# Performance work log

Measured on AMD Instinct MI355X. Metric: run time of the kernel, lower is better.

Reference implementation:

```python
import jax, jax.numpy as jnp
import numpy as np

NS = [65536, 16384, 4096, 1024, 256, 64]          # nodes per level (64 = 8 graphs x 8 dense voxels)
ES = [1048576, 262144, 65536, 16384, 4096]        # edges per level (avg degree 16)
INS = [1, 15, 23, 31, 39]
OUTS = [12, 20, 28, 36, 44]
K = 5                                             # kernel_size


def setup_inputs():
    keys = iter(jax.random.split(jax.random.key(0), 64))
    d = {'x': jax.random.normal(next(keys), (NS[0], 1), jnp.float32),
         'pos': jax.random.uniform(next(keys), (NS[0], 3), jnp.float32)}
    for l in range(5):
        n, e, ci, co = NS[l], ES[l], INS[l], OUTS[l]
        d[f'src{l}'] = jax.random.randint(next(keys), (e,), 0, n)
        d[f'dst{l}'] = jax.random.randint(next(keys), (e,), 0, n)
        d[f'eattr{l}'] = jax.random.normal(next(keys), (e, 3), jnp.float32)
        d[f'cluster{l}'] = jax.random.randint(next(keys), (n,), 0, NS[l + 1])
        d[f'w1_{l}'] = jax.random.normal(next(keys), (3, K), jnp.float32) * 0.5
        d[f'b1_{l}'] = jnp.zeros((K,), jnp.float32)
        d[f'w2_{l}'] = jax.random.normal(next(keys), (K, ci * co), jnp.float32) / np.float32(np.sqrt(K * ci))
        d[f'b2_{l}'] = jnp.zeros((ci * co,), jnp.float32)
        d[f'root_{l}'] = jax.random.normal(next(keys), (ci, co), jnp.float32) / np.float32(np.sqrt(ci))
        d[f'bias_{l}'] = jnp.zeros((co,), jnp.float32)
    d['fc_w'] = jax.random.normal(next(keys), (8 * 47, 10), jnp.float32) / np.float32(np.sqrt(8 * 47))
    d['fc_b'] = jnp.zeros((10,), jnp.float32)
    return d


def _conv(x, src, dst, eattr, w1, b1, w2, b2, root, bias, n):
    # edge-conditioned kernel: MLP(edge_attr) -> [E, ci, co]
    h = jnp.tanh(eattr @ w1 + b1)                                  # [E, K]
    We = (h @ w2 + b2).reshape(eattr.shape[0], x.shape[1], -1)     # [E, ci, co]
    msg = jnp.einsum('ei,eio->eo', x[src], We)                     # gather + per-edge matvec
    s = jax.ops.segment_sum(msg, dst, num_segments=n)
    cnt = jax.ops.segment_sum(jnp.ones((dst.shape[0], 1), x.dtype), dst, num_segments=n)
    agg = s / jnp.maximum(cnt, 1.0)                                # mean aggregation
    return agg + x @ root + bias, jnp.mean(jnp.square(We))


def _pool(x, pos, cluster, n_next):
    # sparse voxel max pool on features, mean on positions; pos concatenated to features
    xm = jax.ops.segment_max(x, cluster, num_segments=n_next)
    xm = jnp.where(jnp.isfinite(xm), xm, 0.0)                      # empty voxels -> 0
    ps = jax.ops.segment_sum(pos, cluster, num_segments=n_next)
    cnt = jax.ops.segment_sum(jnp.ones((pos.shape[0], 1), pos.dtype), cluster, num_segments=n_next)
    pm = ps / jnp.maximum(cnt, 1.0)
    return jnp.concatenate([xm, pm], axis=1), pm


def reference(x, pos, src0, dst0, eattr0, cluster0, w1_0, b1_0, w2_0, b2_0, root_0, bias_0,
              src1, dst1, eattr1, cluster1, w1_1, b1_1, w2_1, b2_1, root_1, bias_1,
              src2, dst2, eattr2, cluster2, w1_2, b1_2, w2_2, b2_2, root_2, bias_2,
              src3, dst3, eattr3, cluster3, w1_3, b1_3, w2_3, b2_3, root_3, bias_3,
              src4, dst4, eattr4, cluster4, w1_4, b1_4, w2_4, b2_4, root_4, bias_4,
              fc_w, fc_b):
    lv = [(src0, dst0, eattr0, cluster0, w1_0, b1_0, w2_0, b2_0, root_0, bias_0),
          (src1, dst1, eattr1, cluster1, w1_1, b1_1, w2_1, b2_1, root_1, bias_1),
          (src2, dst2, eattr2, cluster2, w1_2, b1_2, w2_2, b2_2, root_2, bias_2),
          (src3, dst3, eattr3, cluster3, w1_3, b1_3, w2_3, b2_3, root_3, bias_3),
          (src4, dst4, eattr4, cluster4, w1_4, b1_4, w2_4, b2_4, root_4, bias_4)]
    closs = jnp.float32(0.0)
    for l, (src, dst, ea, cl, w1, b1, w2, b2, rt, bs) in enumerate(lv):
        x, c = _conv(x, src, dst, ea, w1, b1, w2, b2, rt, bs, NS[l])
        closs = closs + c
        x, pos = _pool(x, pos, cl, NS[l + 1])
    feat = x.reshape(-1, 8 * 47)                                   # [B, 8*47]
    logits = feat @ fc_w + fc_b
    return jax.nn.log_softmax(logits, axis=1), closs
```

## Files before the change

kernel.cpp:

```cpp
#include <hip/hip_runtime.h>
#include <hip/hip_fp16.h>
#include <math.h>


#define TILES1 256
#define TSZ1   1024
#define NB1    512
#define NBUK   1024
#define CAP0   1280

__device__ __forceinline__ float ftanh(float x) {
    float e = __expf(2.f * x);
    return 1.f - 2.f / (e + 1.f);
}

__device__ __forceinline__ unsigned fenc(float f) {
    int b = __float_as_int(f);
    return (b < 0) ? ~(unsigned)b : ((unsigned)b | 0x80000000u);
}
__device__ __forceinline__ float fdec(unsigned u) {
    int b = (u & 0x80000000u) ? (int)(u & 0x7fffffffu) : ~(int)u;
    return __int_as_float(b);
}

__device__ __forceinline__ float row_val(const unsigned* __restrict__ row,
                                         int i, int CI) {
    float cn = __uint_as_float(row[CI]);
    if (i < CI - 3) return (cn == 0.f) ? 0.f : fdec(row[i]);
    return __uint_as_float(row[i]) / fmaxf(cn, 1.f);
}

struct Seg4 {
    const int* idx[4];
    int*       cnt[4];
    int*       rp [4];
    int*       out[4];
    int        n  [4];
    int        nb [4];
    int        tstart[5];
};

struct GA {
    const int *src0, *dst0; const float* ea0;
    const int *src1, *dst1; const float* ea1;
    const float *x0, *pos0;
    const int* cluster[5];
    const float *w1[5], *b1[5], *w2[5], *b2[5], *root[5], *bias[5];
    const int* srcE[3]; const float* eaE[3];
    const float *fc_w, *fc_b;
    int* bcnt;
    float4* pay2;
    float* y0;
    float* xn0;
    unsigned* raw[5];
    float* H; float* sq;
    int *M1, *M21, *bktTot, *bs1;
    float4 *pay1, *rec1; int* rp1;
    Seg4 sg;
    float* out;
    const float* hea[4]; int hE[4]; int hb0[5];
    int hsB;
};

__global__ __launch_bounds__(256) void k1_fuseA(GA A)
{
    __shared__ int sh[NBUK];
    int B = blockIdx.x, t = threadIdx.x;

    if (B < 1024) {
        for (int u = t; u < NBUK; u += 256) sh[u] = 0;
        __syncthreads();
        int base = B * 1024 + t;
        int dreg[4];
        #pragma unroll
        for (int it = 0; it < 4; it++) {
            dreg[it] = A.dst0[base + it * 256];
            atomicAdd(&sh[dreg[it] >> 6], 1);
        }
        __syncthreads();
        for (int u = t; u < NBUK; u += 256) {
            int c = sh[u];
            sh[u] = c ? atomicAdd(&A.bcnt[u], c) : 0;
        }
        __syncthreads();
        float w1r[15], b1r[5];
        #pragma unroll
        for (int i = 0; i < 15; i++) w1r[i] = A.w1[0][i];
        #pragma unroll
        for (int i = 0; i < 5; i++)  b1r[i] = A.b1[0][i];
        float acc[20];
        #pragma unroll
        for (int i = 0; i < 20; i++) acc[i] = 0.f;
        #pragma unroll
        for (int it = 0; it < 4; it++) {
            int i = base + it * 256;
            int d = dreg[it];
            int sv = A.src0[i];
            float e0 = A.ea0[i * 3], e1 = A.ea0[i * 3 + 1], e2 = A.ea0[i * 3 + 2];
            float h[5];
            #pragma unroll
            for (int k = 0; k < 5; k++)
                h[k] = ftanh(e0 * w1r[k] + e1 * w1r[5 + k] + e2 * w1r[10 + k] + b1r[k]);
            int p = 5;
            #pragma unroll
            for (int k = 0; k < 5; k++) {
                acc[k] += h[k];
                #pragma unroll
                for (int k2 = k; k2 < 5; k2++) acc[p++] += h[k] * h[k2];
            }
            float xv = A.x0[sv];
            union HU { __half2 h2; float f; } p01, p23;
            p01.h2 = __floats2half2_rn(h[0], h[1]);
            p23.h2 = __floats2half2_rn(h[2], h[3]);
            unsigned wbits = ((unsigned)d << 16) |
                             (unsigned)__half_as_ushort(__float2half_rn(h[4]));
            int bk = d >> 6;
            int ps = atomicAdd(&sh[bk], 1);
            if (ps < CAP0)
                A.pay2[(size_t)bk * CAP0 + ps] =
                    make_float4(xv, p01.f, p23.f, __uint_as_float(wbits));
        }
        __syncthreads();
        float* red = (float*)sh;
        int wid = t >> 6, lane = t & 63;
        #pragma unroll
        for (int v = 0; v < 20; v++) {
            float s = acc[v];
            #pragma unroll
            for (int o = 32; o; o >>= 1) s += __shfl_down(s, o);
            if (lane == 0) red[wid * 20 + v] = s;
        }
        __syncthreads();
        if (t < 20)
            atomicAdd(&A.H[t], red[t] + red[20 + t] + red[40 + t] + red[60 + t]);
        return;
    }
    B -= 1024;
    if (B < TILES1) {
        for (int u = t; u < NB1; u += 256) sh[u] = 0;
        __syncthreads();
        int base = B * TSZ1 + t;
        #pragma unroll
        for (int it = 0; it < 4; it++)
            atomicAdd(&sh[A.dst1[base + it * 256] >> 5], 1);
        __syncthreads();
        for (int u = t; u < NB1; u += 256) {
            int c = sh[u];
            A.M1[(size_t)B * NB1 + u] = c;
            if (c) atomicAdd(&A.bktTot[u], c);
        }
        return;
    }
    B -= TILES1;
    if (B < A.hsB) {
        const int K = 8;
        int j = 0;
        while (j < 3 && B >= A.hb0[j + 1]) j++;
        int bloc = B - A.hb0[j];
        const float* ea = A.hea[j];
        const float* w1p = A.w1[j + 1];
        const float* b1p = A.b1[j + 1];
        float w1r[15], b1r[5];
        #pragma unroll
        for (int i = 0; i < 15; i++) w1r[i] = w1p[i];
        #pragma unroll
        for (int i = 0; i < 5; i++)  b1r[i] = b1p[i];
        float acc[20];
        #pragma unroll
        for (int i = 0; i < 20; i++) acc[i] = 0.f;
        int base = bloc * 256 * K + t;
        for (int it = 0; it < K; it++) {
            int e = base + it * 256;
            if (e < A.hE[j]) {
                float e0 = ea[e * 3], e1 = ea[e * 3 + 1], e2 = ea[e * 3 + 2];
                float h[5];
                #pragma unroll
                for (int k = 0; k < 5; k++)
                    h[k] = ftanh(e0 * w1r[k] + e1 * w1r[5 + k] + e2 * w1r[10 + k] + b1r[k]);
                int p = 5;
                #pragma unroll
                for (int k = 0; k < 5; k++) {
                    acc[k] += h[k];
                    #pragma unroll
                    for (int k2 = k; k2 < 5; k2++) acc[p++] += h[k] * h[k2];
                }
            }
        }
        float* red = (float*)sh;
        int wid = t >> 6, lane = t & 63;
        #pragma unroll
        for (int v = 0; v < 20; v++) {
            float s = acc[v];
            #pragma unroll
            for (int o = 32; o; o >>= 1) s += __shfl_down(s, o);
            if (lane == 0) red[wid * 20 + v] = s;
        }
        __syncthreads();
        if (t < 20)
            atomicAdd(&A.H[(j + 1) * 20 + t],
                      red[t] + red[20 + t] + red[40 + t] + red[60 + t]);
        return;
    }
    B -= A.hsB;
    {
        int s = 0;
        while (s < 3 && B >= A.sg.tstart[s + 1]) s++;
        int i0 = (B - A.sg.tstart[s]) * 1024;
        const int* idx = A.sg.idx[s];
        int* cnt = A.sg.cnt[s];
        int n = A.sg.n[s];
        #pragma unroll
        for (int j = 0; j < 4; j++) {
            int i = i0 + j * 256 + t;
            if (i < n) atomicAdd(&cnt[idx[i]], 1);
        }
    }
}

__global__ __launch_bounds__(256) void k2_fuseB(GA A)
{
    __shared__ int sc[256];
    __shared__ float wsm[96];
    __shared__ float nacc[7 * 64];
    int B = blockIdx.x, t = threadIdx.x;

    if (B < NBUK) {
        if (t < 60) wsm[t] = A.w2[0][t];
        else if (t >= 64  && t < 76)  wsm[60 + t - 64]  = A.b2[0][t - 64];
        else if (t >= 128 && t < 140) wsm[72 + t - 128] = A.root[0][t - 128];
        else if (t >= 192 && t < 204) wsm[84 + t - 192] = A.bias[0][t - 192];
        for (int u = t; u < 7 * 64; u += 256) nacc[u] = 0.f;
        __syncthreads();

        int n = A.bcnt[B];
        if (n > CAP0) n = CAP0;
        size_t base = (size_t)B * CAP0;
        for (int j = t; j < n; j += 256) {
            float4 R = A.pay2[base + j];
            union HU { float f; __half2 h2; } a01, a23;
            a01.f = R.y; a23.f = R.z;
            unsigned wbits = __float_as_uint(R.w);
            int rel = (int)(wbits >> 16) & 63;
            float xv = R.x;
            atomicAdd(&nacc[rel], xv);
            atomicAdd(&nacc[64 + rel],  __low2float(a01.h2)  * xv);
            atomicAdd(&nacc[128 + rel], __high2float(a01.h2) * xv);
            atomicAdd(&nacc[192 + rel], __low2float(a23.h2)  * xv);
            atomicAdd(&nacc[256 + rel], __high2float(a23.h2) * xv);
            atomicAdd(&nacc[320 + rel],
                      __half2float(__ushort_as_half((unsigned short)(wbits & 0xffffu))) * xv);
            atomicAdd(&nacc[384 + rel], 1.f);
        }
        __syncthreads();

        int v0 = B << 6;
        for (int u = t; u < 64 * 12; u += 256) {
            int rel = u / 12, o = u - rel * 12;
            float dg = nacc[384 + rel];
            float inv = 1.f / fmaxf(dg, 1.f);
            float msg = wsm[60 + o] * nacc[rel] + wsm[o] * nacc[64 + rel] +
                        wsm[12 + o] * nacc[128 + rel] + wsm[24 + o] * nacc[192 + rel] +
                        wsm[36 + o] * nacc[256 + rel] + wsm[48 + o] * nacc[320 + rel];
            float xv = A.x0[v0 + rel];
            A.y0[(size_t)(v0 + rel) * 12 + o] =
                msg * inv + xv * wsm[72 + o] + wsm[84 + o];
        }
        return;
    }
    B -= NBUK;
    if (B < NB1) {
        int v = A.M1[(size_t)t * NB1 + B];
        sc[t] = v;
        __syncthreads();
        for (int d = 1; d < 256; d <<= 1) {
            int u = (t >= d) ? sc[t - d] : 0;
            __syncthreads();
            sc[t] += u;
            __syncthreads();
        }
        A.M21[(size_t)t * NB1 + B] = sc[t] - v;
        return;
    }
    B -= NB1;
    if (B < 1) {
        int a0 = A.bktTot[2 * t], a1 = A.bktTot[2 * t + 1];
        int ps = a0 + a1;
        sc[t] = ps;
        __syncthreads();
        for (int d = 1; d < 256; d <<= 1) {
            int u = (t >= d) ? sc[t - d] : 0;
            __syncthreads();
            sc[t] += u;
            __syncthreads();
        }
        int excl = sc[t] - ps;
        A.bs1[2 * t]     = excl;
        A.bs1[2 * t + 1] = excl + a0;
        if (t == 255) A.bs1[512] = sc[255];
        return;
    }
    B -= 1;
    if (B < 4) {
        int s = B;
        int nb = A.sg.nb[s];
        const int* cnt = A.sg.cnt[s];
        int* rp = A.sg.rp[s];
        int VPT = nb >> 8;
        int i0 = t * VPT;
        int sum = 0;
        for (int k = 0; k < VPT; k++) sum += cnt[i0 + k];
        int acc = sum;
        sc[t] = acc;
        __syncthreads();
        for (int d = 1; d < 256; d <<= 1) {
            int t2 = (t >= d) ? sc[t - d] : 0;
            __syncthreads();
            acc += t2;
            sc[t] = acc;
            __syncthreads();
        }
        int running = acc - sum;
        for (int k = 0; k < VPT; k++) {
            rp[i0 + k] = running;
            running += cnt[i0 + k];
        }
        if (t == 255) rp[nb] = running;
        return;
    }
    B -= 4;
    {
        if (t >= 64) return;
        int l = B;
        const float* w2l = A.w2[l];
        const float* b2l = A.b2[l];
        static const int cicoA[5] = {12, 300, 644, 1116, 1716};
        int cico = cicoA[l];
        float d[21];
        #pragma unroll
        for (int i = 0; i < 21; i++) d[i] = 0.f;
        for (int u = t; u < cico; u += 64) {
            float b = b2l[u];
            float w[5];
            #pragma unroll
            for (int k = 0; k < 5; k++) w[k] = w2l[k * cico + u];
            int p = 0;
            #pragma unroll
            for (int k = 0; k < 5; k++) {
                #pragma unroll
                for (int k2 = k; k2 < 5; k2++) d[p++] += w[k] * w[k2];
            }
            #pragma unroll
            for (int k = 0; k < 5; k++) d[15 + k] += b * w[k];
            d[20] += b * b;
        }
        #pragma unroll
        for (int i = 0; i < 21; i++) {
            #pragma unroll
            for (int off = 32; off; off >>= 1) d[i] += __shfl_down(d[i], off);
        }
        if (t == 0) {
            static const int EA[5] = {1048576, 262144, 65536, 16384, 4096};
            const float* H1 = A.H + l * 20;
            const float* H2 = H1 + 5;
            float sq = (float)EA[l] * d[20];
            #pragma unroll
            for (int k = 0; k < 5; k++) sq += 2.f * d[15 + k] * H1[k];
            int p = 0;
            #pragma unroll
            for (int k = 0; k < 5; k++) {
                #pragma unroll
                for (int k2 = k; k2 < 5; k2++) {
                    sq += ((k == k2) ? 1.f : 2.f) * d[p] * H2[p];
                    p++;
                }
            }
            A.sq[l] = sq;
        }
    }
}

__global__ __launch_bounds__(256) void k3_fuseC(GA A)
{
    __shared__ int shi[NB1];
    int B = blockIdx.x, t = threadIdx.x;

    if (B < TILES1) {
        int tile = B;
        for (int u = t; u < NB1; u += 256)
            shi[u] = A.bs1[u] + A.M21[(size_t)tile * NB1 + u];
        __syncthreads();
        int base = tile * TSZ1 + t;
        #pragma unroll
        for (int it = 0; it < 4; it++) {
            int i = base + it * 256;
            int d = A.dst1[i];
            int key = (d << 16) | A.src1[i];
            float e0 = A.ea1[i * 3], e1 = A.ea1[i * 3 + 1], e2 = A.ea1[i * 3 + 2];
            int ps = atomicAdd(&shi[d >> 5], 1);
            A.pay1[ps] = make_float4(__int_as_float(key), e0, e1, e2);
        }
        return;
    }
    B -= TILES1;
    {
        int s = 0;
        while (s < 3 && B >= A.sg.tstart[s + 1]) s++;
        int i0 = (B - A.sg.tstart[s]) * 1024;
        const int* idx = A.sg.idx[s];
        int* cnt = A.sg.cnt[s];
        const int* rp = A.sg.rp[s];
        int* out = A.sg.out[s];
        int n = A.sg.n[s];
        #pragma unroll
        for (int j = 0; j < 4; j++) {
            int i = i0 + j * 256 + t;
            if (i < n) {
                int d = idx[i];
                int p = atomicSub(&cnt[d], 1) - 1;
                out[rp[d] + p] = i;
            }
        }
    }
}

__global__ __launch_bounds__(256) void k4_fuseD(GA A)
{
    __shared__ int hist[32], cur[32];
    int B = blockIdx.x, t = threadIdx.x;

    if (B < NB1) {
        int b = B;
        int lo = A.bs1[b], hi = A.bs1[b + 1];
        int bin0 = b << 5;
        if (t < 32) hist[t] = 0;
        __syncthreads();
        const float* payw = (const float*)A.pay1;
        for (int j = lo + t; j < hi; j += 256) {
            int rel = (int)(__float_as_uint(payw[4 * j]) >> 16) - bin0;
            atomicAdd(&hist[rel], 1);
        }
        __syncthreads();
        if (t < 32) {
            int v = hist[t];
            int val = v;
            #pragma unroll
            for (int d = 1; d < 32; d <<= 1) {
                int u = __shfl_up(val, d);
                if (t >= d) val += u;
            }
            cur[t] = lo + val - v;
            A.rp1[bin0 + t] = lo + val - v;
            if (b == NB1 - 1 && t == 31) A.rp1[NB1 * 32] = hi;
        }
        __syncthreads();
        for (int j = lo + t; j < hi; j += 256) {
            float4 R = A.pay1[j];
            int rel = (int)(__float_as_uint(R.x) >> 16) - bin0;
            int p = atomicAdd(&cur[rel], 1);
            A.rec1[p] = R;
        }
        return;
    }
    B -= NB1;
    {
        int gt = B * 256 + t;
        if (gt >= 16384 * 15) return;
        int c = gt / 15, o = gt - c * 15;
        int r0 = A.sg.rp[3][c], r1 = A.sg.rp[3][c + 1];
        const int* cnid = A.sg.out[3];
        int d = r1 - r0;
        if (o < 12) {
            float m = -INFINITY;
            for (int j = r0; j < r1; j++)
                m = fmaxf(m, A.y0[(size_t)cnid[j] * 12 + o]);
            if (d == 0 || !isfinite(m)) m = 0.f;
            A.xn0[c * 15 + o] = m;
        } else {
            int k = o - 12;
            float sum = 0.f;
            for (int j = r0; j < r1; j++)
                sum += A.pos0[cnid[j] * 3 + k];
            A.xn0[c * 15 + o] = sum / fmaxf((float)d, 1.f);
        }
    }
}

__global__ __launch_bounds__(256) void k5_conv1(GA A)
{
    constexpr int CI = 15, CO = 20, CH = 48, CICO = CI * CO, RN = 24;
    __shared__ float w1s[20];
    __shared__ float4 recb[CH];
    __shared__ int   svb[CH];
    __shared__ float hb[CH * 6];
    __shared__ float xs[CH * CI];
    __shared__ float Sx[6 * CI];
    __shared__ float xown[CI];

    int t = threadIdx.x, v = blockIdx.x;
    if (t < 20) w1s[t] = (t < 15) ? A.w1[1][t] : A.b1[1][t - 15];
    if (t < CI) xown[t] = A.xn0[v * CI + t];
    int r0 = A.rp1[v], r1 = A.rp1[v + 1];
    int d = r1 - r0;
    float acc = 0.f;

    for (int c0 = r0; c0 < r1; c0 += CH) {
        int cn = min(CH, r1 - c0);
        if (t < cn) {
            float4 R = A.rec1[c0 + t];
            recb[t] = R;
            svb[t]  = (int)(__float_as_uint(R.x) & 0xffffu);
            hb[t * 6] = 1.f;
        }
        __syncthreads();
        if (t < cn * 5) {
            int j = t / 5, k = t % 5;
            float e0 = recb[j].y, e1 = recb[j].z, e2 = recb[j].w;
            hb[j * 6 + 1 + k] =
                ftanh(e0 * w1s[k] + e1 * w1s[5 + k] + e2 * w1s[10 + k] + w1s[15 + k]);
        }
        for (int u = t; u < cn * CI; u += 256) {
            int j = u / CI, i = u - j * CI;
            xs[u] = A.xn0[svb[j] * CI + i];
        }
        __syncthreads();
        if (t < 6 * CI) {
            int i = t / 6, k6 = t - (t / 6) * 6;
            for (int j = 0; j < cn; j++)
                acc += hb[j * 6 + k6] * xs[j * CI + i];
        }
        __syncthreads();
    }

    if (t < 6 * CI) Sx[t] = acc;
    __syncthreads();

    if (t < CO) {
        float m = 0.f;
        const float* w2 = A.w2[1];
        const float* b2 = A.b2[1];
        for (int i = 0; i < CI; i++) {
            m += b2[i * CO + t] * Sx[i * 6];
            #pragma unroll
            for (int k = 0; k < 5; k++)
                m += w2[k * CICO + i * CO + t] * Sx[i * 6 + 1 + k];
        }
        m /= fmaxf((float)d, 1.f);
        for (int i = 0; i < CI; i++) m += xown[i] * A.root[1][i * CO + t];
        m += A.bias[1][t];
        int c = A.cluster[1][v];
        unsigned* orow = A.raw[1] + (size_t)c * RN;
        atomicMax(&orow[t], fenc(m));
        if (t < 3) atomicAdd((float*)&orow[CO + t], xown[CI - 3 + t]);
        if (t == 0) atomicAdd((float*)&orow[CO + 3], 1.f);
    }
}

template<int CI, int CO>
__global__ __launch_bounds__(256) void coopP_k(GA A, int l)
{
    constexpr int CH = 48, CICO = CI * CO, RL = CI + 1, RN = CO + 4;
    __shared__ float w1s[20];
    __shared__ int   eb[CH], svb[CH];
    __shared__ float hb[CH * 6];
    __shared__ float xs[CH * CI];
    __shared__ float Sx[6 * CI];
    __shared__ float xown[CI];

    int t = threadIdx.x, v = blockIdx.x;
    int s = l - 2;
    const unsigned* rin = A.raw[l - 1];
    const int* rp = A.sg.rp[s];
    const int* eid = A.sg.out[s];
    const int* src = A.srcE[s];
    const float* eattr = A.eaE[s];

    if (t < 20) w1s[t] = (t < 15) ? A.w1[l][t] : A.b1[l][t - 15];
    if (t < CI) xown[t] = row_val(rin + (size_t)v * RL, t, CI);
    int r0 = rp[v], r1 = rp[v + 1];
    int d = r1 - r0;
    float acc = 0.f;

    for (int c0 = r0; c0 < r1; c0 += CH) {
        int cn = min(CH, r1 - c0);
        if (t < cn) {
            int e = eid[c0 + t];
            eb[t]  = e;
            svb[t] = src[e];
            hb[t * 6] = 1.f;
        }
        __syncthreads();
        if (t < cn * 5) {
            int j = t / 5, k = t % 5;
            int e = eb[j];
            float e0 = eattr[e * 3], e1 = eattr[e * 3 + 1], e2 = eattr[e * 3 + 2];
            hb[j * 6 + 1 + k] =
                ftanh(e0 * w1s[k] + e1 * w1s[5 + k] + e2 * w1s[10 + k] + w1s[15 + k]);
        }
        for (int u = t; u < cn * CI; u += 256) {
            int j = u / CI, i = u - j * CI;
            xs[u] = row_val(rin + (size_t)svb[j] * RL, i, CI);
        }
        __syncthreads();
        if (t < 6 * CI) {
            int i = t / 6, k6 = t - (t / 6) * 6;
            for (int j = 0; j < cn; j++)
                acc += hb[j * 6 + k6] * xs[j * CI + i];
        }
        __syncthreads();
    }

    if (t < 6 * CI) Sx[t] = acc;
    __syncthreads();

    if (t < CO) {
        float m = 0.f;
        const float* w2 = A.w2[l];
        const float* b2 = A.b2[l];
        for (int i = 0; i < CI; i++) {
            m += b2[i * CO + t] * Sx[i * 6];
            #pragma unroll
            for (int k = 0; k < 5; k++)
                m += w2[k * CICO + i * CO + t] * Sx[i * 6 + 1 + k];
        }
        m /= fmaxf((float)d, 1.f);
        for (int i = 0; i < CI; i++) m += xown[i] * A.root[l][i * CO + t];
        m += A.bias[l][t];
        int c = A.cluster[l][v];
        unsigned* orow = A.raw[l] + (size_t)c * RN;
        atomicMax(&orow[t], fenc(m));
        if (t < 3) atomicAdd((float*)&orow[CO + t], xown[CI - 3 + t]);
        if (t == 0) atomicAdd((float*)&orow[CO + 3], 1.f);
    }
}

__global__ __launch_bounds__(128) void k9_fc(GA A)
{
    __shared__ float feat[8 * 376];
    __shared__ float logit[80];
    __shared__ float roff[8];
    const unsigned* r5 = A.raw[4];
    for (int idx = threadIdx.x; idx < 64 * 47; idx += 128) {
        int n = idx / 47, i = idx - n * 47;
        int b = n >> 3, s = n & 7;
        feat[b * 376 + s * 47 + i] = row_val(r5 + (size_t)n * 48, i, 47);
    }
    __syncthreads();
    int t = threadIdx.x;
    if (t < 80) {
        int b = t / 10, j = t % 10;
        float acc = A.fc_b[j];
        for (int k = 0; k < 376; k++) acc += feat[b * 376 + k] * A.fc_w[k * 10 + j];
        logit[t] = acc;
    }
    __syncthreads();
    if (t < 8) {
        float m = -1e30f;
        for (int j = 0; j < 10; j++) m = fmaxf(m, logit[t * 10 + j]);
        float ssum = 0.f;
        for (int j = 0; j < 10; j++) ssum += expf(logit[t * 10 + j] - m);
        roff[t] = m + logf(ssum);
    }
    __syncthreads();
    if (t < 80) A.out[t] = logit[t] - roff[t / 10];
    if (t == 0) {
        const float* sq = A.sq;
        float closs = 0.f;
        closs += sq[0] * (1.0f / 12582912.0f);
        closs += sq[1] * (1.0f / 78643200.0f);
        closs += sq[2] * (1.0f / 42205184.0f);
        closs += sq[3] * (1.0f / 18284544.0f);
        closs += sq[4] * (1.0f / 7028736.0f);
        A.out[80] = closs;
    }
}


extern "C" void kernel_launch(void* const* d_in, const int* in_sizes, int n_in,
                              void* d_out, int out_size, void* d_ws, size_t ws_size,
                              hipStream_t stream)
{
    static const int NSa[6] = {65536, 16384, 4096, 1024, 256, 64};
    static const int ESa[5] = {1048576, 262144, 65536, 16384, 4096};
    static const int RNa[5] = {16, 24, 32, 40, 48};

    int* wsw = (int*)d_ws;
    size_t off = 0;
    auto alw = [&](size_t n) -> size_t {
        size_t p = off; off += (n + 63) & ~(size_t)63; return p;
    };
    size_t degO[5];
    for (int l = 2; l < 5; l++) degO[l] = alw(NSa[l]);
    size_t cdeg0O = alw(NSa[1]);
    size_t HO   = alw(100);
    size_t bcO  = alw(NBUK);
    size_t btO  = alw(NB1);
    size_t rawO[5];
    for (int l = 1; l < 5; l++) rawO[l] = alw((size_t)NSa[l + 1] * RNa[l]);
    size_t zeroWords = off;
    size_t rpO[5], eidO[5];
    for (int l = 2; l < 5; l++) rpO[l]  = alw(NSa[l] + 1);
    size_t crp0O = alw(NSa[1] + 1);
    for (int l = 2; l < 5; l++) eidO[l] = alw(ESa[l]);
    size_t cnid0O = alw(NSa[0]);
    size_t pay2O = alw((size_t)NBUK * CAP0 * 4);
    size_t y0O   = alw((size_t)NSa[0] * 12);
    size_t xn0O  = alw((size_t)NSa[1] * 15);
    size_t M1O   = alw((size_t)TILES1 * NB1);
    size_t M21O  = alw((size_t)TILES1 * NB1);
    size_t bs1O  = alw(NB1 + 1);
    size_t pay1O = alw((size_t)ESa[1] * 4);
    size_t rec1O = alw((size_t)ESa[1] * 4);
    size_t rp1O  = alw(NSa[1] + 1);
    size_t sqO   = alw(8);

    GA A{};
    A.src0 = (const int*)d_in[2];  A.dst0 = (const int*)d_in[3];
    A.ea0  = (const float*)d_in[4];
    A.src1 = (const int*)d_in[12]; A.dst1 = (const int*)d_in[13];
    A.ea1  = (const float*)d_in[14];
    A.x0   = (const float*)d_in[0];
    A.pos0 = (const float*)d_in[1];
    for (int l = 0; l < 5; l++) {
        A.cluster[l] = (const int*)d_in[5 + 10 * l];
        A.w1[l]   = (const float*)d_in[6 + 10 * l];
        A.b1[l]   = (const float*)d_in[7 + 10 * l];
        A.w2[l]   = (const float*)d_in[8 + 10 * l];
        A.b2[l]   = (const float*)d_in[9 + 10 * l];
        A.root[l] = (const float*)d_in[10 + 10 * l];
        A.bias[l] = (const float*)d_in[11 + 10 * l];
    }
    for (int s = 0; s < 3; s++) {
        A.srcE[s] = (const int*)d_in[2 + 10 * (s + 2)];
        A.eaE[s]  = (const float*)d_in[4 + 10 * (s + 2)];
    }
    A.fc_w = (const float*)d_in[52];
    A.fc_b = (const float*)d_in[53];
    A.bcnt = wsw + bcO;
    A.pay2 = (float4*)(wsw + pay2O);
    A.y0   = (float*)(wsw + y0O);
    A.xn0  = (float*)(wsw + xn0O);
    for (int l = 1; l < 5; l++) A.raw[l] = (unsigned*)(wsw + rawO[l]);
    A.H  = (float*)(wsw + HO);
    A.sq = (float*)(wsw + sqO);
    A.M1 = wsw + M1O; A.M21 = wsw + M21O;
    A.bktTot = wsw + btO; A.bs1 = wsw + bs1O;
    A.pay1 = (float4*)(wsw + pay1O);
    A.rec1 = (float4*)(wsw + rec1O);
    A.rp1  = wsw + rp1O;
    A.out  = (float*)d_out;

    int tiles = 0;
    for (int s = 0; s < 3; s++) {
        int l = s + 2;
        A.sg.idx[s] = (const int*)d_in[3 + 10 * l];
        A.sg.cnt[s] = wsw + degO[l];
        A.sg.rp [s] = wsw + rpO[l];
        A.sg.out[s] = wsw + eidO[l];
        A.sg.n  [s] = ESa[l];
        A.sg.nb [s] = NSa[l];
        A.sg.tstart[s] = tiles;
        tiles += (ESa[l] + 1023) / 1024;
    }
    A.sg.idx[3] = (const int*)d_in[5];
    A.sg.cnt[3] = wsw + cdeg0O;
    A.sg.rp [3] = wsw + crp0O;
    A.sg.out[3] = wsw + cnid0O;
    A.sg.n  [3] = NSa[0];
    A.sg.nb [3] = NSa[1];
    A.sg.tstart[3] = tiles;
    tiles += (NSa[0] + 1023) / 1024;
    A.sg.tstart[4] = tiles;

    int hsB = 0;
    A.hb0[0] = 0;
    for (int j = 0; j < 4; j++) {
        A.hea[j] = (const float*)d_in[4 + 10 * (j + 1)];
        A.hE[j]  = ESa[j + 1];
        hsB += (ESa[j + 1] + 2047) / 2048;
        A.hb0[j + 1] = hsB;
    }
    A.hsB = hsB;

    hipMemsetAsync(d_ws, 0, zeroWords * 4, stream);

    k1_fuseA<<<1024 + TILES1 + hsB + tiles, 256, 0, stream>>>(A);
    k2_fuseB<<<NBUK + NB1 + 1 + 4 + 5,      256, 0, stream>>>(A);
    k3_fuseC<<<TILES1 + tiles,              256, 0, stream>>>(A);
    k4_fuseD<<<NB1 + 960,                   256, 0, stream>>>(A);
    k5_conv1<<<NSa[1],                      256, 0, stream>>>(A);
    coopP_k<23, 28><<<NSa[2],               256, 0, stream>>>(A, 2);
    coopP_k<31, 36><<<NSa[3],               256, 0, stream>>>(A, 3);
    coopP_k<39, 44><<<NSa[4],               256, 0, stream>>>(A, 4);
    k9_fc<<<1, 128, 0, stream>>>(A);
}
```

Measured before the change: 415.2 us.

## Stage edge bucketing in LDS and coalesce scatter for levels zero and one

Level-0 edge records are now bucketed into 256 coarser buckets: each block prefix-sums local bucket counts and stages records in shared memory, then writes them as contiguous runs instead of scattering one record at a time. Level 1 drops the separate count/prefix/scatter passes (M1, M21, bktTot) and uses the same single-pass local-staging bucketing. It also computes level-1 MLP statistics there and does a per-bucket LDS counting sort in k3. This removes global passes and uncoalesced scatters, at the cost of large shared-memory use, which may cut occupancy, and fixed-capacity buckets that can silently drop edges on overflow.

```diff
diff --git a/kernel.cpp b/kernel.cpp
--- a/kernel.cpp
+++ b/kernel.cpp
@@ -3,11 +3,14 @@
 #include <math.h>
 
 
-#define TILES1 256
-#define TSZ1   1024
-#define NB1    512
-#define NBUK   1024
-#define CAP0   1280
+#define NT0   512
+#define TSZ0  2048
+#define NBK0  256
+#define CAP0  4608
+#define NT1   128
+#define TSZ1  2048
+#define NBK1  256
+#define CAP1  1280
 
 __device__ __forceinline__ float ftanh(float x) {
     float e = __expf(2.f * x);
@@ -48,41 +51,51 @@
     const float *w1[5], *b1[5], *w2[5], *b2[5], *root[5], *bias[5];
     const int* srcE[3]; const float* eaE[3];
     const float *fc_w, *fc_b;
-    int* bcnt;
-    float4* pay2;
-    float* y0;
-    float* xn0;
+    int *bcnt, *bcnt1;
+    float4 *pay2, *pay1, *rec1;
+    float *y0, *xn0;
     unsigned* raw[5];
-    float* H; float* sq;
-    int *M1, *M21, *bktTot, *bs1;
-    float4 *pay1, *rec1; int* rp1;
+    float *H, *sq;
+    int *bs1, *rp1;
     Seg4 sg;
     float* out;
-    const float* hea[4]; int hE[4]; int hb0[5];
-    int hsB;
+    int hb0[4], hsB;
 };
 
 __global__ __launch_bounds__(256) void k1_fuseA(GA A)
 {
-    __shared__ int sh[NBUK];
+    __shared__ float4 stg[TSZ0];
+    __shared__ unsigned char bkb[TSZ0];
+    __shared__ int hb_[256], gb_[256], ls_[256], cu_[256];
+
     int B = blockIdx.x, t = threadIdx.x;
 
-    if (B < 1024) {
-        for (int u = t; u < NBUK; u += 256) sh[u] = 0;
-        __syncthreads();
-        int base = B * 1024 + t;
-        int dreg[4];
-        #pragma unroll
-        for (int it = 0; it < 4; it++) {
-            dreg[it] = A.dst0[base + it * 256];
-            atomicAdd(&sh[dreg[it] >> 6], 1);
-        }
-        __syncthreads();
-        for (int u = t; u < NBUK; u += 256) {
-            int c = sh[u];
-            sh[u] = c ? atomicAdd(&A.bcnt[u], c) : 0;
-        }
-        __syncthreads();
+    if (B < NT0) {
+        hb_[t] = 0;
+        __syncthreads();
+        int base = B * TSZ0 + t;
+        int dreg[8];
+        #pragma unroll
+        for (int k = 0; k < 8; k++) {
+            dreg[k] = A.dst0[base + k * 256];
+            atomicAdd(&hb_[dreg[k] >> 8], 1);
+        }
+        __syncthreads();
+        int c = hb_[t];
+        gb_[t] = c ? atomicAdd(&A.bcnt[t], c) : 0;
+        ls_[t] = c;
+        __syncthreads();
+        for (int d = 1; d < 256; d <<= 1) {
+            int u = (t >= d) ? ls_[t - d] : 0;
+            __syncthreads();
+            ls_[t] += u;
+            __syncthreads();
+        }
+        int ex = ls_[t] - c;
+        ls_[t] = ex;
+        cu_[t] = ex;
+        __syncthreads();
+
         float w1r[15], b1r[5];
         #pragma unroll
         for (int i = 0; i < 15; i++) w1r[i] = A.w1[0][i];
@@ -92,21 +105,21 @@
         #pragma unroll
         for (int i = 0; i < 20; i++) acc[i] = 0.f;
         #pragma unroll
-        for (int it = 0; it < 4; it++) {
-            int i = base + it * 256;
-            int d = dreg[it];
+        for (int k = 0; k < 8; k++) {
+            int i = base + k * 256;
+            int d = dreg[k];
             int sv = A.src0[i];
             float e0 = A.ea0[i * 3], e1 = A.ea0[i * 3 + 1], e2 = A.ea0[i * 3 + 2];
             float h[5];
             #pragma unroll
-            for (int k = 0; k < 5; k++)
-                h[k] = ftanh(e0 * w1r[k] + e1 * w1r[5 + k] + e2 * w1r[10 + k] + b1r[k]);
+            for (int q = 0; q < 5; q++)
+                h[q] = ftanh(e0 * w1r[q] + e1 * w1r[5 + q] + e2 * w1r[10 + q] + b1r[q]);
             int p = 5;
             #pragma unroll
-            for (int k = 0; k < 5; k++) {
-                acc[k] += h[k];
+            for (int q = 0; q < 5; q++) {
+                acc[q] += h[q];
                 #pragma unroll
-                for (int k2 = k; k2 < 5; k2++) acc[p++] += h[k] * h[k2];
+                for (int q2 = q; q2 < 5; q2++) acc[p++] += h[q] * h[q2];
             }
             float xv = A.x0[sv];
             union HU { __half2 h2; float f; } p01, p23;
@@ -114,14 +127,22 @@
             p23.h2 = __floats2half2_rn(h[2], h[3]);
             unsigned wbits = ((unsigned)d << 16) |
                              (unsigned)__half_as_ushort(__float2half_rn(h[4]));
-            int bk = d >> 6;
-            int ps = atomicAdd(&sh[bk], 1);
-            if (ps < CAP0)
-                A.pay2[(size_t)bk * CAP0 + ps] =
-                    make_float4(xv, p01.f, p23.f, __uint_as_float(wbits));
-        }
-        __syncthreads();
-        float* red = (float*)sh;
+            int bk = d >> 8;
+            int ps = atomicAdd(&cu_[bk], 1);
+            stg[ps] = make_float4(xv, p01.f, p23.f, __uint_as_float(wbits));
+            bkb[ps] = (unsigned char)bk;
+        }
+        __syncthreads();
+        #pragma unroll
+        for (int k = 0; k < 8; k++) {
+            int p = k * 256 + t;
+            int bk = bkb[p];
+            int off = gb_[bk] + (p - ls_[bk]);
+            if (off < CAP0)
+                A.pay2[(size_t)bk * CAP0 + off] = stg[p];
+        }
+        __syncthreads();
+        float* red = (float*)cu_;
         int wid = t >> 6, lane = t & 63;
         #pragma unroll
         for (int v = 0; v < 20; v++) {
@@ -135,31 +156,98 @@
             atomicAdd(&A.H[t], red[t] + red[20 + t] + red[40 + t] + red[60 + t]);
         return;
     }
-    B -= 1024;
-    if (B < TILES1) {
-        for (int u = t; u < NB1; u += 256) sh[u] = 0;
+    B -= NT0;
+    if (B < NT1) {
+        hb_[t] = 0;
         __syncthreads();
         int base = B * TSZ1 + t;
-        #pragma unroll
-        for (int it = 0; it < 4; it++)
-            atomicAdd(&sh[A.dst1[base + it * 256] >> 5], 1);
-        __syncthreads();
-        for (int u = t; u < NB1; u += 256) {
-            int c = sh[u];
-            A.M1[(size_t)B * NB1 + u] = c;
-            if (c) atomicAdd(&A.bktTot[u], c);
-        }
+        int dreg[8];
+        #pragma unroll
+        for (int k = 0; k < 8; k++) {
+            dreg[k] = A.dst1[base + k * 256];
+            atomicAdd(&hb_[dreg[k] >> 6], 1);
+        }
+        __syncthreads();
+        int c = hb_[t];
+        gb_[t] = c ? atomicAdd(&A.bcnt1[t], c) : 0;
+        ls_[t] = c;
+        __syncthreads();
+        for (int d = 1; d < 256; d <<= 1) {
+            int u = (t >= d) ? ls_[t - d] : 0;
+            __syncthreads();
+            ls_[t] += u;
+            __syncthreads();
+        }
+        int ex = ls_[t] - c;
+        ls_[t] = ex;
+        cu_[t] = ex;
+        __syncthreads();
+
+        float w1r[15], b1r[5];
+        #pragma unroll
+        for (int i = 0; i < 15; i++) w1r[i] = A.w1[1][i];
+        #pragma unroll
+        for (int i = 0; i < 5; i++)  b1r[i] = A.b1[1][i];
+        float acc[20];
+        #pragma unroll
+        for (int i = 0; i < 20; i++) acc[i] = 0.f;
+        #pragma unroll
+        for (int k = 0; k < 8; k++) {
+            int i = base + k * 256;
+            int d = dreg[k];
+            int sv = A.src1[i];
+            float e0 = A.ea1[i * 3], e1 = A.ea1[i * 3 + 1], e2 = A.ea1[i * 3 + 2];
+            float h[5];
+            #pragma unroll
+            for (int q = 0; q < 5; q++)
+                h[q] = ftanh(e0 * w1r[q] + e1 * w1r[5 + q] + e2 * w1r[10 + q] + b1r[q]);
+            int p = 5;
+            #pragma unroll
+            for (int q = 0; q < 5; q++) {
+                acc[q] += h[q];
+                #pragma unroll
+                for (int q2 = q; q2 < 5; q2++) acc[p++] += h[q] * h[q2];
+            }
+            int bk = d >> 6;
+            int ps = atomicAdd(&cu_[bk], 1);
+            stg[ps] = make_float4(__int_as_float((d << 16) | sv), e0, e1, e2);
+            bkb[ps] = (unsigned char)bk;
+        }
+        __syncthreads();
+        #pragma unroll
+        for (int k = 0; k < 8; k++) {
+            int p = k * 256 + t;
+            int bk = bkb[p];
+            int off = gb_[bk] + (p - ls_[bk]);
+            if (off < CAP1)
+                A.pay1[(size_t)bk * CAP1 + off] = stg[p];
+        }
+        __syncthreads();
+        float* red = (float*)cu_;
+        int wid = t >> 6, lane = t & 63;
+        #pragma unroll
+        for (int v = 0; v < 20; v++) {
+            float s = acc[v];
+            #pragma unroll
+            for (int o = 32; o; o >>= 1) s += __shfl_down(s, o);
+            if (lane == 0) red[wid * 20 + v] = s;
+        }
+        __syncthreads();
+        if (t < 20)
+            atomicAdd(&A.H[20 + t], red[t] + red[20 + t] + red[40 + t] + red[60 + t]);
         return;
     }
-    B -= TILES1;
+    B -= NT1;
     if (B < A.hsB) {
         const int K = 8;
         int j = 0;
-        while (j < 3 && B >= A.hb0[j + 1]) j++;
+        while (j < 2 && B >= A.hb0[j + 1]) j++;
         int bloc = B - A.hb0[j];
-        const float* ea = A.hea[j];
-        const float* w1p = A.w1[j + 1];
-        const float* b1p = A.b1[j + 1];
+        const float* ea = A.eaE[j];
+        const float* w1p = A.w1[j + 2];
+        const float* b1p = A.b1[j + 2];
+        static const int EJ[3] = {65536, 16384, 4096};
+        int Ej = EJ[j];
         float w1r[15], b1r[5];
         #pragma unroll
         for (int i = 0; i < 15; i++) w1r[i] = w1p[i];
@@ -171,22 +259,22 @@
         int base = bloc * 256 * K + t;
         for (int it = 0; it < K; it++) {
             int e = base + it * 256;
-            if (e < A.hE[j]) {
+            if (e < Ej) {
                 float e0 = ea[e * 3], e1 = ea[e * 3 + 1], e2 = ea[e * 3 + 2];
                 float h[5];
                 #pragma unroll
-                for (int k = 0; k < 5; k++)
-                    h[k] = ftanh(e0 * w1r[k] + e1 * w1r[5 + k] + e2 * w1r[10 + k] + b1r[k]);
+                for (int q = 0; q < 5; q++)
+                    h[q] = ftanh(e0 * w1r[q] + e1 * w1r[5 + q] + e2 * w1r[10 + q] + b1r[q]);
                 int p = 5;
                 #pragma unroll
-                for (int k = 0; k < 5; k++) {
-                    acc[k] += h[k];
+                for (int q = 0; q < 5; q++) {
+                    acc[q] += h[q];
                     #pragma unroll
-                    for (int k2 = k; k2 < 5; k2++) acc[p++] += h[k] * h[k2];
+                    for (int q2 = q; q2 < 5; q2++) acc[p++] += h[q] * h[q2];
                 }
             }
         }
-        float* red = (float*)sh;
+        float* red = (float*)hb_;
         int wid = t >> 6, lane = t & 63;
         #pragma unroll
         for (int v = 0; v < 20; v++) {
@@ -197,7 +285,7 @@
         }
         __syncthreads();
         if (t < 20)
-            atomicAdd(&A.H[(j + 1) * 20 + t],
+            atomicAdd(&A.H[(j + 2) * 20 + t],
                       red[t] + red[20 + t] + red[40 + t] + red[60 + t]);
         return;
     }
@@ -219,17 +307,17 @@
 
 __global__ __launch_bounds__(256) void k2_fuseB(GA A)
 {
+    __shared__ float wsm[96];
+    __shared__ float nacc[7 * NBK0];
     __shared__ int sc[256];
-    __shared__ float wsm[96];
-    __shared__ float nacc[7 * 64];
     int B = blockIdx.x, t = threadIdx.x;
 
-    if (B < NBUK) {
+    if (B < NBK0) {
         if (t < 60) wsm[t] = A.w2[0][t];
         else if (t >= 64  && t < 76)  wsm[60 + t - 64]  = A.b2[0][t - 64];
         else if (t >= 128 && t < 140) wsm[72 + t - 128] = A.root[0][t - 128];
         else if (t >= 192 && t < 204) wsm[84 + t - 192] = A.bias[0][t - 192];
-        for (int u = t; u < 7 * 64; u += 256) nacc[u] = 0.f;
+        for (int u = t; u < 7 * NBK0; u += 256) nacc[u] = 0.f;
         __syncthreads();
 
         int n = A.bcnt[B];
@@ -240,37 +328,38 @@
             union HU { float f; __half2 h2; } a01, a23;
             a01.f = R.y; a23.f = R.z;
             unsigned wbits = __float_as_uint(R.w);
-            int rel = (int)(wbits >> 16) & 63;
+            int rel = (int)(wbits >> 16) & 255;
             float xv = R.x;
             atomicAdd(&nacc[rel], xv);
-            atomicAdd(&nacc[64 + rel],  __low2float(a01.h2)  * xv);
-            atomicAdd(&nacc[128 + rel], __high2float(a01.h2) * xv);
-            atomicAdd(&nacc[192 + rel], __low2float(a23.h2)  * xv);
-            atomicAdd(&nacc[256 + rel], __high2float(a23.h2) * xv);
-            atomicAdd(&nacc[320 + rel],
+            atomicAdd(&nacc[256 + rel],  __low2float(a01.h2)  * xv);
+            atomicAdd(&nacc[512 + rel],  __high2float(a01.h2) * xv);
+            atomicAdd(&nacc[768 + rel],  __low2float(a23.h2)  * xv);
+            atomicAdd(&nacc[1024 + rel], __high2float(a23.h2) * xv);
+            atomicAdd(&nacc[1280 + rel],
                       __half2float(__ushort_as_half((unsigned short)(wbits & 0xffffu))) * xv);
-            atomicAdd(&nacc[384 + rel], 1.f);
-        }
-        __syncthreads();
-
-        int v0 = B << 6;
-        for (int u = t; u < 64 * 12; u += 256) {
+            atomicAdd(&nacc[1536 + rel], 1.f);
+        }
+        __syncthreads();
+
+        int v0 = B << 8;
+        for (int u = t; u < NBK0 * 12; u += 256) {
             int rel = u / 12, o = u - rel * 12;
-            float dg = nacc[384 + rel];
+            float dg = nacc[1536 + rel];
             float inv = 1.f / fmaxf(dg, 1.f);
-            float msg = wsm[60 + o] * nacc[rel] + wsm[o] * nacc[64 + rel] +
-                        wsm[12 + o] * nacc[128 + rel] + wsm[24 + o] * nacc[192 + rel] +
-                        wsm[36 + o] * nacc[256 + rel] + wsm[48 + o] * nacc[320 + rel];
+            float msg = wsm[60 + o] * nacc[rel] + wsm[o] * nacc[256 + rel] +
+                        wsm[12 + o] * nacc[512 + rel] + wsm[24 + o] * nacc[768 + rel] +
+                        wsm[36 + o] * nacc[1024 + rel] + wsm[48 + o] * nacc[1280 + rel];
             float xv = A.x0[v0 + rel];
             A.y0[(size_t)(v0 + rel) * 12 + o] =
                 msg * inv + xv * wsm[72 + o] + wsm[84 + o];
         }
         return;
     }
-    B -= NBUK;
-    if (B < NB1) {
-        int v = A.M1[(size_t)t * NB1 + B];
-        sc[t] = v;
+    B -= NBK0;
+    if (B < 1) {
+        int c = A.bcnt1[t];
+        if (c > CAP1) c = CAP1;
+        sc[t] = c;
         __syncthreads();
         for (int d = 1; d < 256; d <<= 1) {
             int u = (t >= d) ? sc[t - d] : 0;
@@ -278,25 +367,8 @@
             sc[t] += u;
             __syncthreads();
         }
-        A.M21[(size_t)t * NB1 + B] = sc[t] - v;
-        return;
-    }
-    B -= NB1;
-    if (B < 1) {
-        int a0 = A.bktTot[2 * t], a1 = A.bktTot[2 * t + 1];
-        int ps = a0 + a1;
-        sc[t] = ps;
-        __syncthreads();
-        for (int d = 1; d < 256; d <<= 1) {
-            int u = (t >= d) ? sc[t - d] : 0;
-            __syncthreads();
-            sc[t] += u;
-            __syncthreads();
-        }
-        int excl = sc[t] - ps;
-        A.bs1[2 * t]     = excl;
-        A.bs1[2 * t + 1] = excl + a0;
-        if (t == 255) A.bs1[512] = sc[255];
+        A.bs1[t] = sc[t] - c;
+        if (t == 255) { A.bs1[256] = sc[255]; A.rp1[16384] = sc[255]; }
         return;
     }
     B -= 1;
@@ -381,28 +453,12 @@
 
 __global__ __launch_bounds__(256) void k3_fuseC(GA A)
 {
-    __shared__ int shi[NB1];
+    __shared__ float4 st4[CAP1];
+    __shared__ short  inv[CAP1];
+    __shared__ int h64[64], l64[64], c64[64];
     int B = blockIdx.x, t = threadIdx.x;
 
-    if (B < TILES1) {
-        int tile = B;
-        for (int u = t; u < NB1; u += 256)
-            shi[u] = A.bs1[u] + A.M21[(size_t)tile * NB1 + u];
-        __syncthreads();
-        int base = tile * TSZ1 + t;
-        #pragma unroll
-        for (int it = 0; it < 4; it++) {
-            int i = base + it * 256;
-            int d = A.dst1[i];
-            int key = (d << 16) | A.src1[i];
-            float e0 = A.ea1[i * 3], e1 = A.ea1[i * 3 + 1], e2 = A.ea1[i * 3 + 2];
-            int ps = atomicAdd(&shi[d >> 5], 1);
-            A.pay1[ps] = make_float4(__int_as_float(key), e0, e1, e2);
-        }
-        return;
-    }
-    B -= TILES1;
-    {
+    if (B < A.sg.tstart[4]) {
         int s = 0;
         while (s < 3 && B >= A.sg.tstart[s + 1]) s++;
         int i0 = (B - A.sg.tstart[s]) * 1024;
@@ -420,68 +476,67 @@
                 out[rp[d] + p] = i;
             }
         }
-    }
-}
-
-__global__ __launch_bounds__(256) void k4_fuseD(GA A)
-{
-    __shared__ int hist[32], cur[32];
-    int B = blockIdx.x, t = threadIdx.x;
-
-    if (B < NB1) {
+        return;
+    }
+    B -= A.sg.tstart[4];
+    {
         int b = B;
-        int lo = A.bs1[b], hi = A.bs1[b + 1];
-        int bin0 = b << 5;
-        if (t < 32) hist[t] = 0;
-        __syncthreads();
-        const float* payw = (const float*)A.pay1;
-        for (int j = lo + t; j < hi; j += 256) {
-            int rel = (int)(__float_as_uint(payw[4 * j]) >> 16) - bin0;
-            atomicAdd(&hist[rel], 1);
-        }
-        __syncthreads();
-        if (t < 32) {
-            int v = hist[t];
+        int n = A.bcnt1[b];
+        if (n > CAP1) n = CAP1;
+        size_t base = (size_t)b * CAP1;
+        for (int j = t; j < n; j += 256) st4[j] = A.pay1[base + j];
+        if (t < 64) h64[t] = 0;
+        __syncthreads();
+        for (int j = t; j < n; j += 256) {
+            int rel = (int)(__float_as_uint(st4[j].x) >> 16) & 63;
+            atomicAdd(&h64[rel], 1);
+        }
+        __syncthreads();
+        if (t < 64) {
+            int v = h64[t];
             int val = v;
             #pragma unroll
-            for (int d = 1; d < 32; d <<= 1) {
+            for (int d = 1; d < 64; d <<= 1) {
                 int u = __shfl_up(val, d);
                 if (t >= d) val += u;
             }
-            cur[t] = lo + val - v;
-            A.rp1[bin0 + t] = lo + val - v;
-            if (b == NB1 - 1 && t == 31) A.rp1[NB1 * 32] = hi;
-        }
-        __syncthreads();
-        for (int j = lo + t; j < hi; j += 256) {
-            float4 R = A.pay1[j];
-            int rel = (int)(__float_as_uint(R.x) >> 16) - bin0;
-            int p = atomicAdd(&cur[rel], 1);
-            A.rec1[p] = R;
-        }
-        return;
-    }
-    B -= NB1;
-    {
-        int gt = B * 256 + t;
-        if (gt >= 16384 * 15) return;
-        int c = gt / 15, o = gt - c * 15;
-        int r0 = A.sg.rp[3][c], r1 = A.sg.rp[3][c + 1];
-        const int* cnid = A.sg.out[3];
-        int d = r1 - r0;
-        if (o < 12) {
-            float m = -INFINITY;
-            for (int j = r0; j < r1; j++)
-                m = fmaxf(m, A.y0[(size_t)cnid[j] * 12 + o]);
-            if (d == 0 || !isfinite(m)) m = 0.f;
-            A.xn0[c * 15 + o] = m;
-        } else {
-            int k = o - 12;
-            float sum = 0.f;
-            for (int j = r0; j < r1; j++)
-                sum += A.pos0[cnid[j] * 3 + k];
-            A.xn0[c * 15 + o] = sum / fmaxf((float)d, 1.f);
-        }
+            l64[t] = val - v;
+            c64[t] = val - v;
+        }
+        __syncthreads();
+        for (int j = t; j < n; j += 256) {
+            int rel = (int)(__float_as_uint(st4[j].x) >> 16) & 63;
+            int p = atomicAdd(&c64[rel], 1);
+            inv[p] = (short)j;
+        }
+        __syncthreads();
+        int lo = A.bs1[b];
+        for (int j = t; j < n; j += 256)
+            A.rec1[lo + j] = st4[inv[j]];
+        if (t < 64) A.rp1[(b << 6) + t] = lo + l64[t];
+    }
+}
+
+__global__ __launch_bounds__(256) void k4_pool0(GA A)
+{
+    int gt = blockIdx.x * 256 + threadIdx.x;
+    if (gt >= 16384 * 15) return;
+    int c = gt / 15, o = gt - c * 15;
+    int r0 = A.sg.rp[3][c], r1 = A.sg.rp[3][c + 1];
+    const int* cnid = A.sg.out[3];
+    int d = r1 - r0;
+    if (o < 12) {
+        float m = -INFINITY;
+        for (int j = r0; j < r1; j++)
+            m = fmaxf(m, A.y0[(size_t)cnid[j] * 12 + o]);
+        if (d == 0 || !isfinite(m)) m = 0.f;
+        A.xn0[c * 15 + o] = m;
+    } else {
+        int k = o - 12;
+        float sum = 0.f;
+        for (int j = r0; j < r1; j++)
+            sum += A.pos0[cnid[j] * 3 + k];
+        A.xn0[c * 15 + o] = sum / fmaxf((float)d, 1.f);
     }
 }
 
@@ -691,9 +746,9 @@
     size_t degO[5];
     for (int l = 2; l < 5; l++) degO[l] = alw(NSa[l]);
     size_t cdeg0O = alw(NSa[1]);
-    size_t HO   = alw(100);
-    size_t bcO  = alw(NBUK);
-    size_t btO  = alw(NB1);
+    size_t HO    = alw(100);
+    size_t bcO   = alw(NBK0);
+    size_t bc1O  = alw(NBK1);
     size_t rawO[5];
     for (int l = 1; l < 5; l++) rawO[l] = alw((size_t)NSa[l + 1] * RNa[l]);
     size_t zeroWords = off;
@@ -702,13 +757,11 @@
     size_t crp0O = alw(NSa[1] + 1);
     for (int l = 2; l < 5; l++) eidO[l] = alw(ESa[l]);
     size_t cnid0O = alw(NSa[0]);
-    size_t pay2O = alw((size_t)NBUK * CAP0 * 4);
+    size_t pay2O = alw((size_t)NBK0 * CAP0 * 4);
     size_t y0O   = alw((size_t)NSa[0] * 12);
     size_t xn0O  = alw((size_t)NSa[1] * 15);
-    size_t M1O   = alw((size_t)TILES1 * NB1);
-    size_t M21O  = alw((size_t)TILES1 * NB1);
-    size_t bs1O  = alw(NB1 + 1);
-    size_t pay1O = alw((size_t)ESa[1] * 4);
+    size_t bs1O  = alw(NBK1 + 1);
+    size_t pay1O = alw((size_t)NBK1 * CAP1 * 4);
     size_t rec1O = alw((size_t)ESa[1] * 4);
     size_t rp1O  = alw(NSa[1] + 1);
     size_t sqO   = alw(8);
@@ -735,19 +788,19 @@
     }
     A.fc_w = (const float*)d_in[52];
     A.fc_b = (const float*)d_in[53];
-    A.bcnt = wsw + bcO;
+    A.bcnt  = wsw + bcO;
+    A.bcnt1 = wsw + bc1O;
     A.pay2 = (float4*)(wsw + pay2O);
+    A.pay1 = (float4*)(wsw + pay1O);
+    A.rec1 = (float4*)(wsw + rec1O);
     A.y0   = (float*)(wsw + y0O);
     A.xn0  = (float*)(wsw + xn0O);
     for (int l = 1; l < 5; l++) A.raw[l] = (unsigned*)(wsw + rawO[l]);
     A.H  = (float*)(wsw + HO);
     A.sq = (float*)(wsw + sqO);
-    A.M1 = wsw + M1O; A.M21 = wsw + M21O;
-    A.bktTot = wsw + btO; A.bs1 = wsw + bs1O;
-    A.pay1 = (float4*)(wsw + pay1O);
-    A.rec1 = (float4*)(wsw + rec1O);
-    A.rp1  = wsw + rp1O;
-    A.out  = (float*)d_out;
+    A.bs1 = wsw + bs1O;
+    A.rp1 = wsw + rp1O;
+    A.out = (float*)d_out;
 
     int tiles = 0;
     for (int s = 0; s < 3; s++) {
@@ -773,23 +826,21 @@
 
     int hsB = 0;
     A.hb0[0] = 0;
-    for (int j = 0; j < 4; j++) {
-        A.hea[j] = (const float*)d_in[4 + 10 * (j + 1)];
-        A.hE[j]  = ESa[j + 1];
-        hsB += (ESa[j + 1] + 2047) / 2048;
+    for (int j = 0; j < 3; j++) {
+        hsB += (ESa[j + 2] + 2047) / 2048;
         A.hb0[j + 1] = hsB;
     }
     A.hsB = hsB;
 
     hipMemsetAsync(d_ws, 0, zeroWords * 4, stream);
 
-    k1_fuseA<<<1024 + TILES1 + hsB + tiles, 256, 0, stream>>>(A);
-    k2_fuseB<<<NBUK + NB1 + 1 + 4 + 5,      256, 0, stream>>>(A);
-    k3_fuseC<<<TILES1 + tiles,              256, 0, stream>>>(A);
-    k4_fuseD<<<NB1 + 960,                   256, 0, stream>>>(A);
-    k5_conv1<<<NSa[1],                      256, 0, stream>>>(A);
-    coopP_k<23, 28><<<NSa[2],               256, 0, stream>>>(A, 2);
-    coopP_k<31, 36><<<NSa[3],               256, 0, stream>>>(A, 3);
-    coopP_k<39, 44><<<NSa[4],               256, 0, stream>>>(A, 4);
+    k1_fuseA<<<NT0 + NT1 + hsB + tiles, 256, 0, stream>>>(A);
+    k2_fuseB<<<NBK0 + 1 + 4 + 5,        256, 0, stream>>>(A);
+    k3_fuseC<<<tiles + NBK1,            256, 0, stream>>>(A);
+    k4_pool0<<<(16384 * 15 + 255) / 256, 256, 0, stream>>>(A);
+    k5_conv1<<<NSa[1],                  256, 0, stream>>>(A);
+    coopP_k<23, 28><<<NSa[2],           256, 0, stream>>>(A, 2);
+    coopP_k<31, 36><<<NSa[3],           256, 0, stream>>>(A, 3);
+    coopP_k<39, 44><<<NSa[4],           256, 0, stream>>>(A, 4);
     k9_fc<<<1, 128, 0, stream>>>(A);
 }
```

Measured after the change: 378.2 us. 1.1x faster.
